# Optimization experiments

Hardware: AMD Instinct MI355X
Metric: run time of the kernel (lower is better)

The kernel has to match this reference:

```python
import jax, jax.numpy as jnp
import numpy as np

DIM = 1024
NUM_EXPERTS = 8
ACTIVE_EXPERTS = 2
EXPERT_DIM = 2048


def setup_inputs() -> dict:
    key = jax.random.key(0)
    k1, k2, k3, k4 = jax.random.split(key, 4)
    x = jax.random.normal(k1, (1, 2048, DIM), dtype=jnp.float32)
    gate_w = jax.random.normal(k2, (NUM_EXPERTS, DIM), dtype=jnp.float32) * 0.02
    balance_bias = jnp.zeros((NUM_EXPERTS,), dtype=jnp.float32)
    w1 = jax.random.normal(k3, (NUM_EXPERTS, EXPERT_DIM, DIM), dtype=jnp.float32) * 0.02
    w2 = jax.random.normal(k4, (NUM_EXPERTS, DIM, EXPERT_DIM), dtype=jnp.float32) * 0.02
    return {"x": x, "gate_w": gate_w, "balance_bias": balance_bias, "w1": w1, "w2": w2}


def reference(x, gate_w, balance_bias, w1, w2):
    B, S, D = x.shape
    T = B * S
    xf = x.reshape(T, D)
    # gating: sigmoid scores with load-balance bias, then top-k
    gate_logits = jnp.einsum('td,ed->te', xf, gate_w)
    gate_scores = jax.nn.sigmoid(gate_logits + balance_bias)
    topk_scores, topk_idx = jax.lax.top_k(gate_scores, ACTIVE_EXPERTS)
    topk_scores = topk_scores / (topk_scores.sum(axis=-1, keepdims=True) + 1e-6)
    # scatter normalized scores into dense combine weights [T, E]
    comb = jnp.zeros((T, NUM_EXPERTS), dtype=x.dtype)
    comb = comb.at[jnp.arange(T)[:, None], topk_idx].add(topk_scores)
    # expert FFNs (dense over experts; combine weight zeroes unselected)
    h = jax.nn.silu(jnp.einsum('td,ehd->teh', xf, w1))   # [T, E, expert_dim]
    expert_out = jnp.einsum('teh,edh->ted', h, w2)        # [T, E, D]
    out = jnp.einsum('te,ted->td', comb, expert_out)
    return out.reshape(B, S, D)
```

## Files before the change

### kernel.cpp

```cpp
#include <hip/hip_runtime.h>

#define T 2048
#define DIM 1024
#define NE 8
#define ED 2048
#define NSLOT (T * 2)
#define KSPLIT 2
#define WTOT (NE * ED * DIM)

#define BM 128
#define BN 128
#define BK 32

typedef __attribute__((ext_vector_type(8))) short s8v;
typedef __attribute__((ext_vector_type(4))) float f32x4;

__device__ __forceinline__ short f2bf(float f) {
    union { float f; unsigned u; } v;
    v.f = f;
    unsigned r = 0x7FFFu + ((v.u >> 16) & 1u);
    v.u += r;
    return (short)(v.u >> 16);
}

__device__ __forceinline__ float bf2f(short s) {
    union { unsigned u; float f; } v;
    v.u = ((unsigned)(unsigned short)s) << 16;
    return v.f;
}

__device__ __forceinline__ void glds16(const void* g, void* l) {
    __builtin_amdgcn_global_load_lds(
        (const __attribute__((address_space(1))) void*)g,
        (__attribute__((address_space(3))) void*)l, 16, 0, 0);
}

__global__ __launch_bounds__(256) void convert_w_kernel(
    const float* __restrict__ w1, const float* __restrict__ w2,
    short* __restrict__ w1b, short* __restrict__ w2b) {
    size_t c = (size_t)blockIdx.x * 256 + threadIdx.x;
    const float* p1 = w1 + c * 8;
    const float* p2 = w2 + c * 8;
    float4 a0 = *(const float4*)(p1);
    float4 a1 = *(const float4*)(p1 + 4);
    float4 b0 = *(const float4*)(p2);
    float4 b1 = *(const float4*)(p2 + 4);
    s8v o1 = { f2bf(a0.x), f2bf(a0.y), f2bf(a0.z), f2bf(a0.w),
               f2bf(a1.x), f2bf(a1.y), f2bf(a1.z), f2bf(a1.w) };
    s8v o2 = { f2bf(b0.x), f2bf(b0.y), f2bf(b0.z), f2bf(b0.w),
               f2bf(b1.x), f2bf(b1.y), f2bf(b1.z), f2bf(b1.w) };
    *(s8v*)(w1b + c * 8) = o1;
    *(s8v*)(w2b + c * 8) = o2;
}

__global__ void router_kernel(const float* __restrict__ x,
                              const float* __restrict__ gw,
                              const float* __restrict__ bias,
                              short* __restrict__ xb,
                              int* __restrict__ counts,
                              int* __restrict__ top2i,
                              float* __restrict__ top2w) {
    int wid = threadIdx.x >> 6;
    int lane = threadIdx.x & 63;
    int t = blockIdx.x * 4 + wid;

    const float* xr = x + (size_t)t * DIM + lane * 16;
    float4 xv[4];
#pragma unroll
    for (int j = 0; j < 4; ++j) xv[j] = *(const float4*)(xr + j * 4);

    s8v o0, o1;
#pragma unroll
    for (int j = 0; j < 2; ++j) {
        o0[j * 4 + 0] = f2bf(xv[j].x); o0[j * 4 + 1] = f2bf(xv[j].y);
        o0[j * 4 + 2] = f2bf(xv[j].z); o0[j * 4 + 3] = f2bf(xv[j].w);
        o1[j * 4 + 0] = f2bf(xv[j + 2].x); o1[j * 4 + 1] = f2bf(xv[j + 2].y);
        o1[j * 4 + 2] = f2bf(xv[j + 2].z); o1[j * 4 + 3] = f2bf(xv[j + 2].w);
    }
    *(s8v*)(xb + (size_t)t * DIM + lane * 16) = o0;
    *(s8v*)(xb + (size_t)t * DIM + lane * 16 + 8) = o1;

    float sc[NE];
#pragma unroll
    for (int e = 0; e < NE; ++e) {
        const float* gr = gw + e * DIM + lane * 16;
        float p = 0.f;
#pragma unroll
        for (int j = 0; j < 4; ++j) {
            float4 g = *(const float4*)(gr + j * 4);
            p += xv[j].x * g.x + xv[j].y * g.y + xv[j].z * g.z + xv[j].w * g.w;
        }
#pragma unroll
        for (int off = 32; off; off >>= 1) p += __shfl_xor(p, off, 64);
        sc[e] = 1.f / (1.f + __expf(-(p + bias[e])));
    }
    int b0 = 0; float s0 = sc[0];
#pragma unroll
    for (int e = 1; e < NE; ++e) if (sc[e] > s0) { s0 = sc[e]; b0 = e; }
    int b1 = -1; float s1 = -1e30f;
#pragma unroll
    for (int e = 0; e < NE; ++e) if (e != b0 && sc[e] > s1) { s1 = sc[e]; b1 = e; }
    float inv = 1.f / (s0 + s1 + 1e-6f);
    if (lane == 0) {
        top2i[t * 2 + 0] = b0; top2i[t * 2 + 1] = b1;
        top2w[t * 2 + 0] = s0 * inv; top2w[t * 2 + 1] = s1 * inv;
        atomicAdd(&counts[b0], 1);
        atomicAdd(&counts[b1], 1);
    }
}

__global__ __launch_bounds__(256) void plan_kernel(
    const int* __restrict__ counts, const int* __restrict__ top2i,
    int* __restrict__ offsets, int* __restrict__ tok_list, int* __restrict__ slot_of) {
    __shared__ int soff[NE];
    __shared__ int srun[NE];
    if (threadIdx.x == 0) {
        int a = 0;
        for (int e = 0; e < NE; ++e) { soff[e] = a; offsets[e] = a; a += counts[e]; srun[e] = 0; }
    }
    __syncthreads();
    for (int t = threadIdx.x; t < T; t += 256) {
#pragma unroll
        for (int k = 0; k < 2; ++k) {
            int e = top2i[t * 2 + k];
            int pos = atomicAdd(&srun[e], 1);
            int slot = soff[e] + pos;
            tok_list[slot] = t;
            slot_of[t * 2 + k] = slot;
        }
    }
}

__global__ __launch_bounds__(256) void ffn1_kernel(
    const short* __restrict__ xb, const short* __restrict__ w1b,
    const int* __restrict__ counts, const int* __restrict__ offsets,
    const int* __restrict__ tok_list, short* __restrict__ h) {
    int e = blockIdx.z;
    int cnt = counts[e];
    int m0 = blockIdx.y * BM;
    if (m0 >= cnt) return;
    int off = offsets[e];
    int n0 = blockIdx.x * BN;

    __shared__ __align__(16) short As[4][BM][8];
    __shared__ __align__(16) short Bs[4][BN][8];

    int tid = threadIdx.x;
    int lane = tid & 63, w = tid >> 6;
    int mo = (w >> 1) * 64, no = (w & 1) * 64;
    int lrow = lane & 15, lq = lane >> 4;

    f32x4 acc[4][4];
#pragma unroll
    for (int mi = 0; mi < 4; ++mi)
#pragma unroll
        for (int ni = 0; ni < 4; ++ni) acc[mi][ni] = (f32x4){0.f, 0.f, 0.f, 0.f};

    int ra0 = m0 + lane;      if (ra0 > cnt - 1) ra0 = cnt - 1;
    int ra1 = m0 + 64 + lane; if (ra1 > cnt - 1) ra1 = cnt - 1;
    const short* a0 = xb + (size_t)tok_list[off + ra0] * DIM + w * 8;
    const short* a1 = xb + (size_t)tok_list[off + ra1] * DIM + w * 8;
    const short* b0 = w1b + ((size_t)e * ED + n0 + lane) * DIM + w * 8;
    const short* b1 = b0 + (size_t)64 * DIM;
    short* lA0 = &As[w][0][0];
    short* lA1 = &As[w][64][0];
    short* lB0 = &Bs[w][0][0];
    short* lB1 = &Bs[w][64][0];

    for (int k0 = 0; k0 < DIM; k0 += BK) {
        __syncthreads();
        glds16(a0 + k0, lA0);
        glds16(a1 + k0, lA1);
        glds16(b0 + k0, lB0);
        glds16(b1 + k0, lB1);
        __syncthreads();
        s8v af[4], bf[4];
#pragma unroll
        for (int mi = 0; mi < 4; ++mi) af[mi] = *(const s8v*)&As[lq][mo + mi * 16 + lrow][0];
#pragma unroll
        for (int ni = 0; ni < 4; ++ni) bf[ni] = *(const s8v*)&Bs[lq][no + ni * 16 + lrow][0];
#pragma unroll
        for (int mi = 0; mi < 4; ++mi)
#pragma unroll
            for (int ni = 0; ni < 4; ++ni)
                acc[mi][ni] = __builtin_amdgcn_mfma_f32_16x16x32_bf16(af[mi], bf[ni], acc[mi][ni], 0, 0, 0);
    }

#pragma unroll
    for (int mi = 0; mi < 4; ++mi) {
#pragma unroll
        for (int ni = 0; ni < 4; ++ni) {
            int ln = n0 + no + ni * 16 + lrow;
#pragma unroll
            for (int r = 0; r < 4; ++r) {
                int row = m0 + mo + mi * 16 + lq * 4 + r;
                if (row < cnt) {
                    float v = acc[mi][ni][r];
                    v = v / (1.f + __expf(-v));
                    h[(size_t)(off + row) * ED + ln] = f2bf(v);
                }
            }
        }
    }
}

__global__ __launch_bounds__(256) void ffn2_kernel(
    const short* __restrict__ h, const short* __restrict__ w2b,
    const int* __restrict__ counts, const int* __restrict__ offsets,
    short* __restrict__ eo) {
    int z = blockIdx.z;
    int e = z >> 1, ks = z & 1;
    int cnt = counts[e];
    int m0 = blockIdx.y * BM;
    if (m0 >= cnt) return;
    int off = offsets[e];
    int n0 = blockIdx.x * BN;
    const int kbase = ks * (ED / KSPLIT);

    __shared__ __align__(16) short As[4][BM][8];
    __shared__ __align__(16) short Bs[4][BN][8];

    int tid = threadIdx.x;
    int lane = tid & 63, w = tid >> 6;
    int mo = (w >> 1) * 64, no = (w & 1) * 64;
    int lrow = lane & 15, lq = lane >> 4;

    f32x4 acc[4][4];
#pragma unroll
    for (int mi = 0; mi < 4; ++mi)
#pragma unroll
        for (int ni = 0; ni < 4; ++ni) acc[mi][ni] = (f32x4){0.f, 0.f, 0.f, 0.f};

    int ra0 = m0 + lane;      if (ra0 > cnt - 1) ra0 = cnt - 1;
    int ra1 = m0 + 64 + lane; if (ra1 > cnt - 1) ra1 = cnt - 1;
    const short* a0 = h + (size_t)(off + ra0) * ED + kbase + w * 8;
    const short* a1 = h + (size_t)(off + ra1) * ED + kbase + w * 8;
    const short* b0 = w2b + ((size_t)e * DIM + n0 + lane) * ED + kbase + w * 8;
    const short* b1 = b0 + (size_t)64 * ED;
    short* lA0 = &As[w][0][0];
    short* lA1 = &As[w][64][0];
    short* lB0 = &Bs[w][0][0];
    short* lB1 = &Bs[w][64][0];

    for (int k0 = 0; k0 < ED / KSPLIT; k0 += BK) {
        __syncthreads();
        glds16(a0 + k0, lA0);
        glds16(a1 + k0, lA1);
        glds16(b0 + k0, lB0);
        glds16(b1 + k0, lB1);
        __syncthreads();
        s8v af[4], bf[4];
#pragma unroll
        for (int mi = 0; mi < 4; ++mi) af[mi] = *(const s8v*)&As[lq][mo + mi * 16 + lrow][0];
#pragma unroll
        for (int ni = 0; ni < 4; ++ni) bf[ni] = *(const s8v*)&Bs[lq][no + ni * 16 + lrow][0];
#pragma unroll
        for (int mi = 0; mi < 4; ++mi)
#pragma unroll
            for (int ni = 0; ni < 4; ++ni)
                acc[mi][ni] = __builtin_amdgcn_mfma_f32_16x16x32_bf16(af[mi], bf[ni], acc[mi][ni], 0, 0, 0);
    }

    short* eop = eo + (size_t)ks * NSLOT * DIM;
#pragma unroll
    for (int mi = 0; mi < 4; ++mi) {
#pragma unroll
        for (int ni = 0; ni < 4; ++ni) {
            int ln = n0 + no + ni * 16 + lrow;
#pragma unroll
            for (int r = 0; r < 4; ++r) {
                int row = m0 + mo + mi * 16 + lq * 4 + r;
                if (row < cnt) {
                    eop[(size_t)(off + row) * DIM + ln] = f2bf(acc[mi][ni][r]);
                }
            }
        }
    }
}

__global__ __launch_bounds__(256) void combine_kernel(
    const short* __restrict__ eo, const int* __restrict__ slot_of,
    const float* __restrict__ top2w, float* __restrict__ out) {
    int idx = blockIdx.x * 256 + threadIdx.x;
    int t = idx >> 7;
    int c = idx & 127;
    int s0 = slot_of[2 * t], s1 = slot_of[2 * t + 1];
    float w0 = top2w[2 * t], w1 = top2w[2 * t + 1];
    const short* e0 = eo;
    const short* e1 = eo + (size_t)NSLOT * DIM;
    s8v a0 = *(const s8v*)(e0 + (size_t)s0 * DIM + c * 8);
    s8v a1 = *(const s8v*)(e1 + (size_t)s0 * DIM + c * 8);
    s8v b0 = *(const s8v*)(e0 + (size_t)s1 * DIM + c * 8);
    s8v b1 = *(const s8v*)(e1 + (size_t)s1 * DIM + c * 8);
    float4 o[2];
#pragma unroll
    for (int j = 0; j < 8; ++j) {
        float v = w0 * (bf2f(a0[j]) + bf2f(a1[j])) + w1 * (bf2f(b0[j]) + bf2f(b1[j]));
        ((float*)o)[j] = v;
    }
    float4* op = (float4*)(out + (size_t)t * DIM + c * 8);
    op[0] = o[0];
    op[1] = o[1];
}

extern "C" void kernel_launch(void* const* d_in, const int* in_sizes, int n_in,
                              void* d_out, int out_size, void* d_ws, size_t ws_size,
                              hipStream_t stream) {
    const float* x    = (const float*)d_in[0];
    const float* gw   = (const float*)d_in[1];
    const float* bias = (const float*)d_in[2];
    const float* w1   = (const float*)d_in[3];
    const float* w2   = (const float*)d_in[4];
    float* out = (float*)d_out;

    char* ws = (char*)d_ws;
    short* xb  = (short*)ws;
    short* h   = (short*)(ws + (4ull << 20));
    short* w1b = (short*)(ws + (20ull << 20));
    short* eo  = (short*)(ws + (20ull << 20));
    short* w2b = (short*)(ws + (52ull << 20));
    char* meta = ws + (84ull << 20);
    int*   counts   = (int*)(meta);
    int*   offsets  = (int*)(meta + 64);
    int*   tok_list = (int*)(meta + 128);
    int*   slot_of  = (int*)(meta + 128 + 4 * NSLOT);
    int*   top2i    = (int*)(meta + 128 + 8 * NSLOT);
    float* top2w    = (float*)(meta + 128 + 8 * NSLOT + 8 * T);

    hipMemsetAsync(counts, 0, 32, stream);

    convert_w_kernel<<<WTOT / 8 / 256, 256, 0, stream>>>(w1, w2, w1b, w2b);
    router_kernel<<<T / 4, 256, 0, stream>>>(x, gw, bias, xb, counts, top2i, top2w);
    plan_kernel<<<1, 256, 0, stream>>>(counts, top2i, offsets, tok_list, slot_of);
    ffn1_kernel<<<dim3(ED / BN, T / BM, NE), 256, 0, stream>>>(xb, w1b, counts, offsets, tok_list, h);
    ffn2_kernel<<<dim3(DIM / BN, T / BM, NE * KSPLIT), 256, 0, stream>>>(h, w2b, counts, offsets, eo);
    combine_kernel<<<T * DIM / 8 / 256, 256, 0, stream>>>(eo, slot_of, top2w, out);
}
```

Before: 337.7 us.

## Double-buffer LDS in expert GEMMs, compact tile worklist, fuse convert with router

Both expert GEMM kernels now use two LDS buffers. The next K-tile is prefetched with global_load_lds while MFMAs run on the current one, which cuts the barriers per iteration from two to one. The plan kernel builds a compact list of (expert, M-tile) pairs, so the GEMM grids cover only real tiles instead of launching many blocks that exit immediately. The weight conversion and router kernels are merged into one launch to remove a launch and let the two overlap. In exchange, LDS use per block doubles, which may lower occupancy.

```diff
diff --git a/kernel.cpp b/kernel.cpp
--- a/kernel.cpp
+++ b/kernel.cpp
@@ -7,10 +7,12 @@
 #define NSLOT (T * 2)
 #define KSPLIT 2
 #define WTOT (NE * ED * DIM)
+#define CONVBLK (WTOT / 8 / 256)
 
 #define BM 128
 #define BN 128
 #define BK 32
+#define MAXWL 40
 
 typedef __attribute__((ext_vector_type(8))) short s8v;
 typedef __attribute__((ext_vector_type(4))) float f32x4;
@@ -35,34 +37,32 @@
         (__attribute__((address_space(3))) void*)l, 16, 0, 0);
 }
 
-__global__ __launch_bounds__(256) void convert_w_kernel(
+__global__ __launch_bounds__(256) void prep_kernel(
     const float* __restrict__ w1, const float* __restrict__ w2,
-    short* __restrict__ w1b, short* __restrict__ w2b) {
-    size_t c = (size_t)blockIdx.x * 256 + threadIdx.x;
-    const float* p1 = w1 + c * 8;
-    const float* p2 = w2 + c * 8;
-    float4 a0 = *(const float4*)(p1);
-    float4 a1 = *(const float4*)(p1 + 4);
-    float4 b0 = *(const float4*)(p2);
-    float4 b1 = *(const float4*)(p2 + 4);
-    s8v o1 = { f2bf(a0.x), f2bf(a0.y), f2bf(a0.z), f2bf(a0.w),
-               f2bf(a1.x), f2bf(a1.y), f2bf(a1.z), f2bf(a1.w) };
-    s8v o2 = { f2bf(b0.x), f2bf(b0.y), f2bf(b0.z), f2bf(b0.w),
-               f2bf(b1.x), f2bf(b1.y), f2bf(b1.z), f2bf(b1.w) };
-    *(s8v*)(w1b + c * 8) = o1;
-    *(s8v*)(w2b + c * 8) = o2;
-}
-
-__global__ void router_kernel(const float* __restrict__ x,
-                              const float* __restrict__ gw,
-                              const float* __restrict__ bias,
-                              short* __restrict__ xb,
-                              int* __restrict__ counts,
-                              int* __restrict__ top2i,
-                              float* __restrict__ top2w) {
+    short* __restrict__ w1b, short* __restrict__ w2b,
+    const float* __restrict__ x, const float* __restrict__ gw,
+    const float* __restrict__ bias, short* __restrict__ xb,
+    int* __restrict__ counts, int* __restrict__ top2i, float* __restrict__ top2w) {
+    int bx = blockIdx.x;
+    if (bx < CONVBLK) {
+        size_t c = (size_t)bx * 256 + threadIdx.x;
+        const float* p1 = w1 + c * 8;
+        const float* p2 = w2 + c * 8;
+        float4 a0 = *(const float4*)(p1);
+        float4 a1 = *(const float4*)(p1 + 4);
+        float4 b0 = *(const float4*)(p2);
+        float4 b1 = *(const float4*)(p2 + 4);
+        s8v o1 = { f2bf(a0.x), f2bf(a0.y), f2bf(a0.z), f2bf(a0.w),
+                   f2bf(a1.x), f2bf(a1.y), f2bf(a1.z), f2bf(a1.w) };
+        s8v o2 = { f2bf(b0.x), f2bf(b0.y), f2bf(b0.z), f2bf(b0.w),
+                   f2bf(b1.x), f2bf(b1.y), f2bf(b1.z), f2bf(b1.w) };
+        *(s8v*)(w1b + c * 8) = o1;
+        *(s8v*)(w2b + c * 8) = o2;
+        return;
+    }
     int wid = threadIdx.x >> 6;
     int lane = threadIdx.x & 63;
-    int t = blockIdx.x * 4 + wid;
+    int t = (bx - CONVBLK) * 4 + wid;
 
     const float* xr = x + (size_t)t * DIM + lane * 16;
     float4 xv[4];
@@ -111,12 +111,19 @@
 
 __global__ __launch_bounds__(256) void plan_kernel(
     const int* __restrict__ counts, const int* __restrict__ top2i,
-    int* __restrict__ offsets, int* __restrict__ tok_list, int* __restrict__ slot_of) {
+    int* __restrict__ offsets, int* __restrict__ tok_list, int* __restrict__ slot_of,
+    int* __restrict__ wl, int* __restrict__ nwl) {
     __shared__ int soff[NE];
     __shared__ int srun[NE];
     if (threadIdx.x == 0) {
         int a = 0;
         for (int e = 0; e < NE; ++e) { soff[e] = a; offsets[e] = a; a += counts[e]; srun[e] = 0; }
+        int n = 0;
+        for (int e = 0; e < NE; ++e) {
+            int mt = (counts[e] + BM - 1) / BM;
+            for (int m = 0; m < mt; ++m) wl[n++] = (e << 16) | m;
+        }
+        *nwl = n;
     }
     __syncthreads();
     for (int t = threadIdx.x; t < T; t += 256) {
@@ -134,16 +141,18 @@
 __global__ __launch_bounds__(256) void ffn1_kernel(
     const short* __restrict__ xb, const short* __restrict__ w1b,
     const int* __restrict__ counts, const int* __restrict__ offsets,
-    const int* __restrict__ tok_list, short* __restrict__ h) {
-    int e = blockIdx.z;
+    const int* __restrict__ tok_list, const int* __restrict__ wl,
+    const int* __restrict__ nwl, short* __restrict__ h) {
+    int my = blockIdx.y;
+    if (my >= *nwl) return;
+    int e = wl[my] >> 16;
+    int m0 = (wl[my] & 0xffff) * BM;
     int cnt = counts[e];
-    int m0 = blockIdx.y * BM;
-    if (m0 >= cnt) return;
     int off = offsets[e];
     int n0 = blockIdx.x * BN;
 
-    __shared__ __align__(16) short As[4][BM][8];
-    __shared__ __align__(16) short Bs[4][BN][8];
+    __shared__ __align__(16) short As[2][4][BM][8];
+    __shared__ __align__(16) short Bs[2][4][BN][8];
 
     int tid = threadIdx.x;
     int lane = tid & 63, w = tid >> 6;
@@ -162,23 +171,31 @@
     const short* a1 = xb + (size_t)tok_list[off + ra1] * DIM + w * 8;
     const short* b0 = w1b + ((size_t)e * ED + n0 + lane) * DIM + w * 8;
     const short* b1 = b0 + (size_t)64 * DIM;
-    short* lA0 = &As[w][0][0];
-    short* lA1 = &As[w][64][0];
-    short* lB0 = &Bs[w][0][0];
-    short* lB1 = &Bs[w][64][0];
-
-    for (int k0 = 0; k0 < DIM; k0 += BK) {
+    short* lA0 = &As[0][w][0][0];
+    short* lA1 = &As[0][w][64][0];
+    short* lB0 = &Bs[0][w][0][0];
+    short* lB1 = &Bs[0][w][64][0];
+    const int BUFO = 4 * BM * 8;
+
+    const int NK = DIM / BK;
+    glds16(a0, lA0); glds16(a1, lA1); glds16(b0, lB0); glds16(b1, lB1);
+
+    for (int kk = 0; kk < NK; ++kk) {
+        int cur = kk & 1;
         __syncthreads();
-        glds16(a0 + k0, lA0);
-        glds16(a1 + k0, lA1);
-        glds16(b0 + k0, lB0);
-        glds16(b1 + k0, lB1);
-        __syncthreads();
+        if (kk + 1 < NK) {
+            int nb = (cur ^ 1) * BUFO;
+            int k0 = (kk + 1) * BK;
+            glds16(a0 + k0, lA0 + nb);
+            glds16(a1 + k0, lA1 + nb);
+            glds16(b0 + k0, lB0 + nb);
+            glds16(b1 + k0, lB1 + nb);
+        }
         s8v af[4], bf[4];
 #pragma unroll
-        for (int mi = 0; mi < 4; ++mi) af[mi] = *(const s8v*)&As[lq][mo + mi * 16 + lrow][0];
-#pragma unroll
-        for (int ni = 0; ni < 4; ++ni) bf[ni] = *(const s8v*)&Bs[lq][no + ni * 16 + lrow][0];
+        for (int mi = 0; mi < 4; ++mi) af[mi] = *(const s8v*)&As[cur][lq][mo + mi * 16 + lrow][0];
+#pragma unroll
+        for (int ni = 0; ni < 4; ++ni) bf[ni] = *(const s8v*)&Bs[cur][lq][no + ni * 16 + lrow][0];
 #pragma unroll
         for (int mi = 0; mi < 4; ++mi)
 #pragma unroll
@@ -207,18 +224,20 @@
 __global__ __launch_bounds__(256) void ffn2_kernel(
     const short* __restrict__ h, const short* __restrict__ w2b,
     const int* __restrict__ counts, const int* __restrict__ offsets,
+    const int* __restrict__ wl, const int* __restrict__ nwl,
     short* __restrict__ eo) {
-    int z = blockIdx.z;
-    int e = z >> 1, ks = z & 1;
+    int my = blockIdx.y;
+    if (my >= *nwl) return;
+    int e = wl[my] >> 16;
+    int m0 = (wl[my] & 0xffff) * BM;
+    int ks = blockIdx.z;
     int cnt = counts[e];
-    int m0 = blockIdx.y * BM;
-    if (m0 >= cnt) return;
     int off = offsets[e];
     int n0 = blockIdx.x * BN;
     const int kbase = ks * (ED / KSPLIT);
 
-    __shared__ __align__(16) short As[4][BM][8];
-    __shared__ __align__(16) short Bs[4][BN][8];
+    __shared__ __align__(16) short As[2][4][BM][8];
+    __shared__ __align__(16) short Bs[2][4][BN][8];
 
     int tid = threadIdx.x;
     int lane = tid & 63, w = tid >> 6;
@@ -237,23 +256,31 @@
     const short* a1 = h + (size_t)(off + ra1) * ED + kbase + w * 8;
     const short* b0 = w2b + ((size_t)e * DIM + n0 + lane) * ED + kbase + w * 8;
     const short* b1 = b0 + (size_t)64 * ED;
-    short* lA0 = &As[w][0][0];
-    short* lA1 = &As[w][64][0];
-    short* lB0 = &Bs[w][0][0];
-    short* lB1 = &Bs[w][64][0];
-
-    for (int k0 = 0; k0 < ED / KSPLIT; k0 += BK) {
+    short* lA0 = &As[0][w][0][0];
+    short* lA1 = &As[0][w][64][0];
+    short* lB0 = &Bs[0][w][0][0];
+    short* lB1 = &Bs[0][w][64][0];
+    const int BUFO = 4 * BM * 8;
+
+    const int NK = (ED / KSPLIT) / BK;
+    glds16(a0, lA0); glds16(a1, lA1); glds16(b0, lB0); glds16(b1, lB1);
+
+    for (int kk = 0; kk < NK; ++kk) {
+        int cur = kk & 1;
         __syncthreads();
-        glds16(a0 + k0, lA0);
-        glds16(a1 + k0, lA1);
-        glds16(b0 + k0, lB0);
-        glds16(b1 + k0, lB1);
-        __syncthreads();
+        if (kk + 1 < NK) {
+            int nb = (cur ^ 1) * BUFO;
+            int k0 = (kk + 1) * BK;
+            glds16(a0 + k0, lA0 + nb);
+            glds16(a1 + k0, lA1 + nb);
+            glds16(b0 + k0, lB0 + nb);
+            glds16(b1 + k0, lB1 + nb);
+        }
         s8v af[4], bf[4];
 #pragma unroll
-        for (int mi = 0; mi < 4; ++mi) af[mi] = *(const s8v*)&As[lq][mo + mi * 16 + lrow][0];
-#pragma unroll
-        for (int ni = 0; ni < 4; ++ni) bf[ni] = *(const s8v*)&Bs[lq][no + ni * 16 + lrow][0];
+        for (int mi = 0; mi < 4; ++mi) af[mi] = *(const s8v*)&As[cur][lq][mo + mi * 16 + lrow][0];
+#pragma unroll
+        for (int ni = 0; ni < 4; ++ni) bf[ni] = *(const s8v*)&Bs[cur][lq][no + ni * 16 + lrow][0];
 #pragma unroll
         for (int mi = 0; mi < 4; ++mi)
 #pragma unroll
@@ -326,13 +353,15 @@
     int*   slot_of  = (int*)(meta + 128 + 4 * NSLOT);
     int*   top2i    = (int*)(meta + 128 + 8 * NSLOT);
     float* top2w    = (float*)(meta + 128 + 8 * NSLOT + 8 * T);
+    int*   wl       = (int*)(meta + 128 + 8 * NSLOT + 16 * T);
+    int*   nwl      = (int*)(meta + 128 + 8 * NSLOT + 16 * T + 4 * MAXWL);
 
     hipMemsetAsync(counts, 0, 32, stream);
 
-    convert_w_kernel<<<WTOT / 8 / 256, 256, 0, stream>>>(w1, w2, w1b, w2b);
-    router_kernel<<<T / 4, 256, 0, stream>>>(x, gw, bias, xb, counts, top2i, top2w);
-    plan_kernel<<<1, 256, 0, stream>>>(counts, top2i, offsets, tok_list, slot_of);
-    ffn1_kernel<<<dim3(ED / BN, T / BM, NE), 256, 0, stream>>>(xb, w1b, counts, offsets, tok_list, h);
-    ffn2_kernel<<<dim3(DIM / BN, T / BM, NE * KSPLIT), 256, 0, stream>>>(h, w2b, counts, offsets, eo);
+    prep_kernel<<<CONVBLK + T / 4, 256, 0, stream>>>(w1, w2, w1b, w2b,
+                                                     x, gw, bias, xb, counts, top2i, top2w);
+    plan_kernel<<<1, 256, 0, stream>>>(counts, top2i, offsets, tok_list, slot_of, wl, nwl);
+    ffn1_kernel<<<dim3(ED / BN, MAXWL), 256, 0, stream>>>(xb, w1b, counts, offsets, tok_list, wl, nwl, h);
+    ffn2_kernel<<<dim3(DIM / BN, MAXWL, KSPLIT), 256, 0, stream>>>(h, w2b, counts, offsets, wl, nwl, eo);
     combine_kernel<<<T * DIM / 8 / 256, 256, 0, stream>>>(eo, slot_of, top2w, out);
 }
```

Result: faster. 326.5 us (-3.3%).
